# Performance work log

Measured on AMD Instinct MI355X. Metric: run time of the kernel, lower is better.

The kernel has to match this reference:

```python
import jax, jax.numpy as jnp
import numpy as np

H = 12          # num_attention_heads
DH = 64         # attention_head_size
EPS = 1e-12     # F.normalize eps
MAX_LOG_SCALE = float(np.log(1.0 / 0.01))  # clamp max for logit_scale


def _l2norm(x):
    # F.normalize(x, dim=-1): x / max(||x||_2, eps)
    n = jnp.sqrt(jnp.sum(x * x, axis=-1, keepdims=True))
    return x / jnp.maximum(n, EPS)


def setup_inputs() -> dict:
    key = jax.random.key(0)
    ks = jax.random.split(key, 9)
    B, S, D = 4, 2048, 768
    sd = 1.0 / np.sqrt(D)
    inp = {
        "hidden_states": jax.random.normal(ks[0], (B, S, D), jnp.float32),
        "Wq": jax.random.normal(ks[1], (D, D), jnp.float32) * sd,
        "bq": jnp.zeros((D,), jnp.float32),
        "Wk": jax.random.normal(ks[2], (D, D), jnp.float32) * sd,
        "bk": jnp.zeros((D,), jnp.float32),
        "Wv": jax.random.normal(ks[3], (D, D), jnp.float32) * sd,
        "bv": jnp.zeros((D,), jnp.float32),
        "Wo": jax.random.normal(ks[4], (D, D), jnp.float32) * sd,
        "bo": jnp.zeros((D,), jnp.float32),
        "logit_scale": jnp.log(10.0 * jnp.ones((H, 1, 1), jnp.float32)),
    }
    return inp


def reference(hidden_states, Wq, bq, Wk, bk, Wv, bv, Wo, bo, logit_scale):
    B, S, D = hidden_states.shape
    # QKV projections (torch Linear: x @ W.T + b), split heads -> [B,H,S,DH]
    def proj(W, b):
        y = hidden_states @ W.T + b
        return y.reshape(B, S, H, DH).transpose(0, 2, 1, 3)
    q = proj(Wq, bq)
    k = proj(Wk, bk)
    v = proj(Wv, bv)
    # cosine-similarity scores scaled by clamped-exp per-head logit scale
    scale = jnp.exp(jnp.minimum(logit_scale, MAX_LOG_SCALE))  # [H,1,1]
    scores = jnp.einsum('bhqd,bhkd->bhqk', _l2norm(q), _l2norm(k)) * scale[None]
    probs = jax.nn.softmax(scores, axis=-1)
    ctx = jnp.einsum('bhqk,bhkd->bhqd', probs, v)
    ctx = ctx.transpose(0, 2, 1, 3).reshape(B, S, D)
    return ctx @ Wo.T + bo
```

## Files before the change

kernel.cpp:

```cpp
#include <hip/hip_runtime.h>
#include <math.h>

#define Hh 12
#define S_LEN 2048
#define D_MODEL 768
#define HD 64

static constexpr float MAXLS = 4.6051701859880914f;
static constexpr float LOG2E = 1.4426950408889634f;

typedef short bf16x8 __attribute__((ext_vector_type(8)));
typedef float f32x4  __attribute__((ext_vector_type(4)));
typedef float f32x16 __attribute__((ext_vector_type(16)));
typedef unsigned short u16x4 __attribute__((ext_vector_type(4)));
typedef unsigned short u16x8 __attribute__((ext_vector_type(8)));
typedef unsigned int u32x4 __attribute__((ext_vector_type(4)));

__device__ __forceinline__ unsigned short f2bf(float x) {
    unsigned int u = __builtin_bit_cast(unsigned int, x);
    unsigned int r = (u + 0x7FFF + ((u >> 16) & 1)) >> 16;
    return (unsigned short)r;
}

__device__ __forceinline__ unsigned int cvtpk(float a, float b) {
    unsigned int r;
    asm("v_cvt_pk_bf16_f32 %0, %1, %2" : "=v"(r) : "v"(a), "v"(b));
    return r;
}

__device__ __forceinline__ void gload16(const void* g, void* l) {
    __builtin_amdgcn_global_load_lds(
        (const __attribute__((address_space(1))) unsigned int*)g,
        (__attribute__((address_space(3))) unsigned int*)l, 16, 0, 0);
}

__global__ __launch_bounds__(256)
void convert_bf16(const float* __restrict__ hs,
                  const float* __restrict__ Wq, const float* __restrict__ Wk,
                  const float* __restrict__ Wv, const float* __restrict__ Wo,
                  unsigned short* __restrict__ hsb,
                  unsigned short* __restrict__ wqkvb,
                  unsigned short* __restrict__ wob)
{
    const long long N0 = 8192LL * 768;
    const long long NW = 768LL * 768;
    const long long e  = ((long long)blockIdx.x * 256 + threadIdx.x) * 8;
    const float* src; unsigned short* dst;
    if (e < N0) { src = hs + e; dst = hsb + e; }
    else if (e < N0 + 3*NW) {
        const long long r = e - N0;
        const int z = (int)(r / NW);
        src = (z == 0 ? Wq : z == 1 ? Wk : Wv) + (r - (long long)z * NW);
        dst = wqkvb + r;
    } else {
        const long long r = e - N0 - 3*NW;
        src = Wo + r; dst = wob + r;
    }
    const float4 f0 = *(const float4*)src;
    const float4 f1 = *(const float4*)(src + 4);
    u16x8 o;
    o[0]=f2bf(f0.x); o[1]=f2bf(f0.y); o[2]=f2bf(f0.z); o[3]=f2bf(f0.w);
    o[4]=f2bf(f1.x); o[5]=f2bf(f1.y); o[6]=f2bf(f1.z); o[7]=f2bf(f1.w);
    *(u16x8*)dst = o;
}

template<int MODE, int BN, int NWGX>
__global__ __launch_bounds__(256)
void gemm_bf16(const unsigned short* __restrict__ A,
               const unsigned short* __restrict__ Wt,
               const float* __restrict__ b0, const float* __restrict__ b1,
               const float* __restrict__ b2, const float* __restrict__ ls,
               unsigned short* __restrict__ qb, unsigned short* __restrict__ kb,
               unsigned short* __restrict__ vt, float* __restrict__ out)
{
    constexpr int K  = 768;
    constexpr int JW = BN / 32;
    __shared__ char As[16384];
    __shared__ char Bs[BN * 128];

    constexpr int CPX = (NWGX * 64) / 8;
    const int bid = blockIdx.x;
    const int wg  = (bid & 7) * CPX + (bid >> 3);
    const int n0  = (wg % NWGX) * BN;
    const int m0  = (wg / NWGX) * 128;

    const int tid = threadIdx.x, w = tid >> 6, l = tid & 63;
    const int wr = w >> 1, wc = w & 1, hi = l >> 4, ll = l & 15;

    const int srow = l >> 3;
    const int sch  = (l & 7) ^ srow;
    const char* Ab = (const char*)(A  + (size_t)(m0 + w*32) * K) + srow * (K*2) + sch * 16;
    const char* Bb = (const char*)(Wt + (size_t)(n0 + w*(BN/4)) * K) + srow * (K*2) + sch * 16;
    char* AsW = As + (w*32) * 128;
    char* BsW = Bs + (w*(BN/4)) * 128;

    f32x4 acc[4][JW];
    #pragma unroll
    for (int i = 0; i < 4; ++i)
        #pragma unroll
        for (int j = 0; j < JW; ++j) acc[i][j] = (f32x4){0.f,0.f,0.f,0.f};

    for (int kt = 0; kt < K/64; ++kt) {
        __syncthreads();
        #pragma unroll
        for (int s = 0; s < 4; ++s)
            gload16(Ab + kt*128 + s*8*(K*2), AsW + s*1024);
        #pragma unroll
        for (int s = 0; s < JW; ++s)
            gload16(Bb + kt*128 + s*8*(K*2), BsW + s*1024);
        __syncthreads();

        bf16x8 af[2][4], bf[2][JW];
        #pragma unroll
        for (int kk = 0; kk < 2; ++kk) {
            const int pc = kk*4 + hi;
            #pragma unroll
            for (int i = 0; i < 4; ++i) {
                const int ra = wr*64 + i*16 + ll;
                af[kk][i] = *(const bf16x8*)(As + ra*128 + ((pc ^ (ra & 7)) << 4));
            }
            #pragma unroll
            for (int j = 0; j < JW; ++j) {
                const int rb = wc*(BN/2) + j*16 + ll;
                bf[kk][j] = *(const bf16x8*)(Bs + rb*128 + ((pc ^ (rb & 7)) << 4));
            }
        }
        #pragma unroll
        for (int kk = 0; kk < 2; ++kk)
            #pragma unroll
            for (int i = 0; i < 4; ++i)
                #pragma unroll
                for (int j = 0; j < JW; ++j)
                    acc[i][j] = __builtin_amdgcn_mfma_f32_16x16x32_bf16(af[kk][i], bf[kk][j], acc[i][j], 0, 0, 0);
    }

    if (MODE == 0) {
        const int z  = n0 / 768;
        const int nl = (n0 % 768) + wc*64;
        const int h  = nl >> 6;
        const int b  = m0 >> 11;
        const int s0 = (m0 & (S_LEN-1)) + wr*64;
        const float* bias = (z == 0) ? b0 : (z == 1) ? b1 : b2;
        float bj[4];
        #pragma unroll
        for (int j = 0; j < 4; ++j) bj[j] = bias[nl + j*16 + ll];

        if (z < 2) {
            const float sc = (z == 0) ? expf(fminf(ls[h], MAXLS)) * LOG2E : 1.0f;
            unsigned short* dst = (z == 0 ? qb : kb) + ((size_t)(b*Hh + h) * S_LEN) * HD;
            #pragma unroll
            for (int i = 0; i < 4; ++i) {
                float vv[4][4]; float ss[4] = {0.f, 0.f, 0.f, 0.f};
                #pragma unroll
                for (int r = 0; r < 4; ++r)
                    #pragma unroll
                    for (int j = 0; j < 4; ++j) {
                        const float x = acc[i][j][r] + bj[j];
                        vv[r][j] = x; ss[r] += x * x;
                    }
                #pragma unroll
                for (int mm = 1; mm < 16; mm <<= 1) {
                    ss[0] += __shfl_xor(ss[0], mm, 64);
                    ss[1] += __shfl_xor(ss[1], mm, 64);
                    ss[2] += __shfl_xor(ss[2], mm, 64);
                    ss[3] += __shfl_xor(ss[3], mm, 64);
                }
                #pragma unroll
                for (int r = 0; r < 4; ++r) {
                    const float inv = sc / fmaxf(sqrtf(ss[r]), 1e-12f);
                    const int s = s0 + i*16 + hi*4 + r;
                    u16x4 o;
                    #pragma unroll
                    for (int j = 0; j < 4; ++j) o[j] = f2bf(vv[r][j] * inv);
                    *(u16x4*)(dst + (size_t)s * HD + ll*4) = o;
                }
            }
        } else {
            __syncthreads();
            char* T = (w < 2 ? As : Bs) + (w & 1) * 8192;
            const int ch_add = hi & 1;
            const int half8  = hi >> 1;
            #pragma unroll
            for (int j = 0; j < 4; ++j) {
                const int d = j*16 + ll;
                #pragma unroll
                for (int i = 0; i < 4; ++i) {
                    u16x4 o;
                    #pragma unroll
                    for (int r = 0; r < 4; ++r) o[r] = f2bf(acc[i][j][r] + bj[j]);
                    const int byteoff = d*128 + (((i*2 + ch_add) ^ (d & 7)) << 4) + half8*8;
                    *(u16x4*)(T + byteoff) = o;
                }
            }
            const int dl = l >> 2;
            #pragma unroll
            for (int dp = 0; dp < 4; ++dp) {
                const int d = dp*16 + dl;
                unsigned short* vrow = vt + ((size_t)(b*Hh + h) * HD + d) * S_LEN + s0;
                #pragma unroll
                for (int rep = 0; rep < 2; ++rep) {
                    const int c = (l & 3) + rep*4;
                    const u16x8 vv = *(const u16x8*)(T + d*128 + ((c ^ (d & 7)) << 4));
                    *(u16x8*)(vrow + c*8) = vv;
                }
            }
        }
    } else {
        #pragma unroll
        for (int i = 0; i < 4; ++i)
            #pragma unroll
            for (int j = 0; j < JW; ++j) {
                const int n = n0 + wc*(BN/2) + j*16 + ll;
                const float bn = b0[n];
                #pragma unroll
                for (int r = 0; r < 4; ++r) {
                    const int m = m0 + wr*64 + i*16 + hi*4 + r;
                    out[(size_t)m * D_MODEL + n] = acc[i][j][r] + bn;
                }
            }
    }
}

__global__ __launch_bounds__(256, 4)
void attn_mfma5(const char* __restrict__ qb_, const char* __restrict__ kb_,
                const char* __restrict__ vtb_,
                unsigned short* __restrict__ ctx)
{
    __shared__ char smem[49152];
    constexpr int NT = S_LEN / 64;

    const int flat = blockIdx.x;
    const int xcd = flat & 7, ix = flat >> 3;
    const int bh = xcd * 6 + (ix >> 4);
    const int q0 = (ix & 15) * 128;
    const int b = bh / Hh, h = bh % Hh;

    const int tid = threadIdx.x, w = tid >> 6, l = tid & 63;
    const int lq = l & 31, g = l >> 5;

    const char* qg = qb_ + ((size_t)bh * S_LEN + q0 + w * 32) * 128;
    const char* kg = kb_ + (size_t)bh * S_LEN * 128 + (size_t)l * 128;
    const char* vg = vtb_ + (size_t)bh * HD * (S_LEN * 2) + (size_t)l * 4096;

    bf16x8 qf[4];
    #pragma unroll
    for (int s = 0; s < 4; ++s)
        qf[s] = *(const bf16x8*)(qg + lq * 128 + s * 32 + g * 16);

    const short oneb = (short)0x3F80;
    const bf16x8 onesf = {oneb, oneb, oneb, oneb, oneb, oneb, oneb, oneb};

    f32x16 acco0, acco1, accl;
    #pragma unroll
    for (int i = 0; i < 16; ++i) { acco0[i] = 0.f; acco1[i] = 0.f; accl[i] = 0.f; }

#define STAGE(bi, kt) do {                                                   \
        char* dstS = smem + ((bi) << 14);                                    \
        gload16(kg + (size_t)(kt) * 8192 + w * 16,        dstS + w * 1024);          \
        gload16(kg + (size_t)(kt) * 8192 + (w+4) * 16,    dstS + (w+4) * 1024);      \
        gload16(vg + (size_t)(kt) * 128 + w * 16,         dstS + 8192 + w * 1024);   \
        gload16(vg + (size_t)(kt) * 128 + (w+4) * 16,     dstS + 8192 + (w+4) * 1024); \
    } while (0)

    auto qk = [&](const char* Ks, f32x16& o0, f32x16& o1) {
        __builtin_amdgcn_s_setprio(1);
        #pragma unroll
        for (int s = 0; s < 4; ++s) {
            const bf16x8 kf0 = *(const bf16x8*)(Ks + (2*s + g) * 1024 + lq * 16);
            o0 = __builtin_amdgcn_mfma_f32_32x32x16_bf16(kf0, qf[s], o0, 0, 0, 0);
            const bf16x8 kf1 = *(const bf16x8*)(Ks + (2*s + g) * 1024 + 512 + lq * 16);
            o1 = __builtin_amdgcn_mfma_f32_32x32x16_bf16(kf1, qf[s], o1, 0, 0, 0);
        }
        __builtin_amdgcn_s_setprio(0);
    };

    auto softmax_pv = [&](const f32x16& s0v, const f32x16& s1v, const char* Vs) {
        #pragma unroll
        for (int t = 0; t < 4; ++t) {
            float p[8];
            #pragma unroll
            for (int e = 0; e < 8; ++e) {
                const float sv = (t & 2) ? s1v[8*(t&1) + e] : s0v[8*(t&1) + e];
                p[e] = __builtin_amdgcn_exp2f(sv);
            }
            u32x4 pu;
            pu[0] = cvtpk(p[0], p[1]);
            pu[1] = cvtpk(p[2], p[3]);
            pu[2] = cvtpk(p[4], p[5]);
            pu[3] = cvtpk(p[6], p[7]);
            const bf16x8 pa = __builtin_bit_cast(bf16x8, pu);

            __builtin_amdgcn_s_setprio(1);
            const bf16x8 vf0 = *(const bf16x8*)(Vs + (2*t + g) * 1024 + lq * 16);
            acco0 = __builtin_amdgcn_mfma_f32_32x32x16_bf16(pa, vf0, acco0, 0, 0, 0);
            const bf16x8 vf1 = *(const bf16x8*)(Vs + (2*t + g) * 1024 + 512 + lq * 16);
            acco1 = __builtin_amdgcn_mfma_f32_32x32x16_bf16(pa, vf1, acco1, 0, 0, 0);
            accl  = __builtin_amdgcn_mfma_f32_32x32x16_bf16(pa, onesf, accl, 0, 0, 0);
            __builtin_amdgcn_s_setprio(0);
        }
    };

    STAGE(0, 0);
    __syncthreads();
    STAGE(1, 1);
    f32x16 sa0c, sa1c;
    #pragma unroll
    for (int i = 0; i < 16; ++i) { sa0c[i] = 0.f; sa1c[i] = 0.f; }
    qk(smem, sa0c, sa1c);
    __syncthreads();

    int bc = 0, bn = 1, bs = 2;
    #pragma unroll 3
    for (int kt = 0; kt < NT - 1; ++kt) {
        if (kt + 2 < NT) STAGE(bs, kt + 2);
        f32x16 sa0n, sa1n;
        #pragma unroll
        for (int i = 0; i < 16; ++i) { sa0n[i] = 0.f; sa1n[i] = 0.f; }
        qk(smem + (bn << 14), sa0n, sa1n);
        softmax_pv(sa0c, sa1c, smem + (bc << 14) + 8192);
        __syncthreads();
        sa0c = sa0n; sa1c = sa1n;
        const int t0 = bc; bc = bn; bn = bs; bs = t0;
    }
    softmax_pv(sa0c, sa1c, smem + (bc << 14) + 8192);
#undef STAGE

    #pragma unroll
    for (int r = 0; r < 16; ++r) {
        const int qrow = (r & 3) + 8 * (r >> 2) + 4 * g;
        const float inv = 1.0f / accl[r];
        unsigned short* crow = ctx + ((size_t)b * S_LEN + q0 + w * 32 + qrow) * D_MODEL + h * HD;
        crow[lq]      = f2bf(acco0[r] * inv);
        crow[32 + lq] = f2bf(acco1[r] * inv);
    }
}

extern "C" void kernel_launch(void* const* d_in, const int* in_sizes, int n_in,
                              void* d_out, int out_size, void* d_ws, size_t ws_size,
                              hipStream_t stream)
{
    const float* hs = (const float*)d_in[0];
    const float* Wq = (const float*)d_in[1];
    const float* bq = (const float*)d_in[2];
    const float* Wk = (const float*)d_in[3];
    const float* bk = (const float*)d_in[4];
    const float* Wv = (const float*)d_in[5];
    const float* bv = (const float*)d_in[6];
    const float* Wo = (const float*)d_in[7];
    const float* bo = (const float*)d_in[8];
    const float* ls = (const float*)d_in[9];
    float* out = (float*)d_out;

    const int B = 4;
    const size_t nHS = 8192ULL * 768;
    const size_t nW  = 768ULL * 768;
    const size_t nPB = (size_t)B * Hh * S_LEN * HD;

    unsigned short* hsb   = (unsigned short*)d_ws;
    unsigned short* wqkvb = hsb + nHS;
    unsigned short* wob   = wqkvb + 3 * nW;
    unsigned short* qbuf  = wob + nW;
    unsigned short* kbuf  = qbuf + nPB;
    unsigned short* vtb   = kbuf + nPB;
    unsigned short* cbuf  = vtb + nPB;

    hipLaunchKernelGGL(convert_bf16, dim3(4224), dim3(256), 0, stream,
                       hs, Wq, Wk, Wv, Wo, hsb, wqkvb, wob);

    hipLaunchKernelGGL((gemm_bf16<0, 128, 18>), dim3(18 * 64), dim3(256), 0, stream,
                       hsb, wqkvb, bq, bk, bv, ls, qbuf, kbuf, vtb, nullptr);

    hipLaunchKernelGGL(attn_mfma5, dim3((S_LEN/128) * B * Hh), dim3(256), 0, stream,
                       (const char*)qbuf, (const char*)kbuf, (const char*)vtb, cbuf);

    hipLaunchKernelGGL((gemm_bf16<1, 64, 12>), dim3(12 * 64), dim3(256), 0, stream,
                       cbuf, wob, bo, nullptr, nullptr, nullptr,
                       nullptr, nullptr, nullptr, out);
}
```

Before: 214.8 us.

## Give each attention wave 64 query rows and compute row sums in VALU

The attention kernel now runs 2 waves of 64 query rows each instead of 4 waves of 32. Each K/V fragment read from LDS therefore feeds twice as many MFMAs. The extra ones-vector MFMA that produced softmax denominators is replaced by VALU sums of the probabilities, combined across lane halves with shuffles. The 3-buffer software pipeline that overlapped the next QK with the current softmax/PV becomes a plain 2-buffer loop. This lowers per-block wave count and register headroom, and may expose more latency.

```diff
diff --git a/kernel.cpp b/kernel.cpp
--- a/kernel.cpp
+++ b/kernel.cpp
@@ -221,12 +221,12 @@
     }
 }
 
-__global__ __launch_bounds__(256, 4)
-void attn_mfma5(const char* __restrict__ qb_, const char* __restrict__ kb_,
+__global__ __launch_bounds__(128, 2)
+void attn_mfma6(const char* __restrict__ qb_, const char* __restrict__ kb_,
                 const char* __restrict__ vtb_,
                 unsigned short* __restrict__ ctx)
 {
-    __shared__ char smem[49152];
+    __shared__ char smem[32768];
     constexpr int NT = S_LEN / 64;
 
     const int flat = blockIdx.x;
@@ -238,100 +238,107 @@
     const int tid = threadIdx.x, w = tid >> 6, l = tid & 63;
     const int lq = l & 31, g = l >> 5;
 
-    const char* qg = qb_ + ((size_t)bh * S_LEN + q0 + w * 32) * 128;
+    const char* qg = qb_ + ((size_t)bh * S_LEN + q0 + w * 64) * 128;
     const char* kg = kb_ + (size_t)bh * S_LEN * 128 + (size_t)l * 128;
     const char* vg = vtb_ + (size_t)bh * HD * (S_LEN * 2) + (size_t)l * 4096;
 
-    bf16x8 qf[4];
+    bf16x8 qf0[4], qf1[4];
     #pragma unroll
-    for (int s = 0; s < 4; ++s)
-        qf[s] = *(const bf16x8*)(qg + lq * 128 + s * 32 + g * 16);
-
-    const short oneb = (short)0x3F80;
-    const bf16x8 onesf = {oneb, oneb, oneb, oneb, oneb, oneb, oneb, oneb};
-
-    f32x16 acco0, acco1, accl;
+    for (int s = 0; s < 4; ++s) {
+        qf0[s] = *(const bf16x8*)(qg + (size_t)lq * 128 + s * 32 + g * 16);
+        qf1[s] = *(const bf16x8*)(qg + (size_t)(32 + lq) * 128 + s * 32 + g * 16);
+    }
+
+    f32x16 acc00, acc01, acc10, acc11;
     #pragma unroll
-    for (int i = 0; i < 16; ++i) { acco0[i] = 0.f; acco1[i] = 0.f; accl[i] = 0.f; }
-
-#define STAGE(bi, kt) do {                                                   \
-        char* dstS = smem + ((bi) << 14);                                    \
-        gload16(kg + (size_t)(kt) * 8192 + w * 16,        dstS + w * 1024);          \
-        gload16(kg + (size_t)(kt) * 8192 + (w+4) * 16,    dstS + (w+4) * 1024);      \
-        gload16(vg + (size_t)(kt) * 128 + w * 16,         dstS + 8192 + w * 1024);   \
-        gload16(vg + (size_t)(kt) * 128 + (w+4) * 16,     dstS + 8192 + (w+4) * 1024); \
+    for (int i = 0; i < 16; ++i) { acc00[i]=0.f; acc01[i]=0.f; acc10[i]=0.f; acc11[i]=0.f; }
+    float lsum0 = 0.f, lsum1 = 0.f;
+
+#define STAGE(bi, kt) do {                                                    \
+        char* dS = smem + ((bi) << 14);                                       \
+        gload16(kg + (size_t)(kt)*8192 + (4*w+0)*16, dS + (4*w+0)*1024);      \
+        gload16(kg + (size_t)(kt)*8192 + (4*w+1)*16, dS + (4*w+1)*1024);      \
+        gload16(kg + (size_t)(kt)*8192 + (4*w+2)*16, dS + (4*w+2)*1024);      \
+        gload16(kg + (size_t)(kt)*8192 + (4*w+3)*16, dS + (4*w+3)*1024);      \
+        gload16(vg + (size_t)(kt)*128 + (4*w+0)*16, dS + 8192 + (4*w+0)*1024);\
+        gload16(vg + (size_t)(kt)*128 + (4*w+1)*16, dS + 8192 + (4*w+1)*1024);\
+        gload16(vg + (size_t)(kt)*128 + (4*w+2)*16, dS + 8192 + (4*w+2)*1024);\
+        gload16(vg + (size_t)(kt)*128 + (4*w+3)*16, dS + 8192 + (4*w+3)*1024);\
     } while (0)
 
-    auto qk = [&](const char* Ks, f32x16& o0, f32x16& o1) {
+    STAGE(0, 0);
+    __syncthreads();
+    int cur = 0;
+
+    for (int kt = 0; kt < NT; ++kt) {
+        if (kt + 1 < NT) STAGE(cur ^ 1, kt + 1);
+        const char* Ks = smem + (cur << 14);
+        const char* Vs = Ks + 8192;
+
+        f32x16 sa00, sa01, sa10, sa11;
+        #pragma unroll
+        for (int i = 0; i < 16; ++i) { sa00[i]=0.f; sa01[i]=0.f; sa10[i]=0.f; sa11[i]=0.f; }
+
         __builtin_amdgcn_s_setprio(1);
         #pragma unroll
         for (int s = 0; s < 4; ++s) {
             const bf16x8 kf0 = *(const bf16x8*)(Ks + (2*s + g) * 1024 + lq * 16);
-            o0 = __builtin_amdgcn_mfma_f32_32x32x16_bf16(kf0, qf[s], o0, 0, 0, 0);
             const bf16x8 kf1 = *(const bf16x8*)(Ks + (2*s + g) * 1024 + 512 + lq * 16);
-            o1 = __builtin_amdgcn_mfma_f32_32x32x16_bf16(kf1, qf[s], o1, 0, 0, 0);
+            sa00 = __builtin_amdgcn_mfma_f32_32x32x16_bf16(kf0, qf0[s], sa00, 0, 0, 0);
+            sa01 = __builtin_amdgcn_mfma_f32_32x32x16_bf16(kf0, qf1[s], sa01, 0, 0, 0);
+            sa10 = __builtin_amdgcn_mfma_f32_32x32x16_bf16(kf1, qf0[s], sa10, 0, 0, 0);
+            sa11 = __builtin_amdgcn_mfma_f32_32x32x16_bf16(kf1, qf1[s], sa11, 0, 0, 0);
         }
         __builtin_amdgcn_s_setprio(0);
-    };
-
-    auto softmax_pv = [&](const f32x16& s0v, const f32x16& s1v, const char* Vs) {
+
         #pragma unroll
         for (int t = 0; t < 4; ++t) {
-            float p[8];
+            float p0[8], p1[8];
             #pragma unroll
             for (int e = 0; e < 8; ++e) {
-                const float sv = (t & 2) ? s1v[8*(t&1) + e] : s0v[8*(t&1) + e];
-                p[e] = __builtin_amdgcn_exp2f(sv);
-            }
-            u32x4 pu;
-            pu[0] = cvtpk(p[0], p[1]);
-            pu[1] = cvtpk(p[2], p[3]);
-            pu[2] = cvtpk(p[4], p[5]);
-            pu[3] = cvtpk(p[6], p[7]);
-            const bf16x8 pa = __builtin_bit_cast(bf16x8, pu);
-
+                const float s0v = (t & 2) ? sa10[8*(t&1) + e] : sa00[8*(t&1) + e];
+                const float s1v = (t & 2) ? sa11[8*(t&1) + e] : sa01[8*(t&1) + e];
+                p0[e] = __builtin_amdgcn_exp2f(s0v);
+                p1[e] = __builtin_amdgcn_exp2f(s1v);
+            }
+            lsum0 += ((p0[0]+p0[1]) + (p0[2]+p0[3])) + ((p0[4]+p0[5]) + (p0[6]+p0[7]));
+            lsum1 += ((p1[0]+p1[1]) + (p1[2]+p1[3])) + ((p1[4]+p1[5]) + (p1[6]+p1[7]));
+            u32x4 u0, u1;
+            u0[0] = cvtpk(p0[0], p0[1]); u0[1] = cvtpk(p0[2], p0[3]);
+            u0[2] = cvtpk(p0[4], p0[5]); u0[3] = cvtpk(p0[6], p0[7]);
+            u1[0] = cvtpk(p1[0], p1[1]); u1[1] = cvtpk(p1[2], p1[3]);
+            u1[2] = cvtpk(p1[4], p1[5]); u1[3] = cvtpk(p1[6], p1[7]);
+            const bf16x8 pa0 = __builtin_bit_cast(bf16x8, u0);
+            const bf16x8 pa1 = __builtin_bit_cast(bf16x8, u1);
+
+            const bf16x8 vf0 = *(const bf16x8*)(Vs + (2*t + g) * 1024 + lq * 16);
+            const bf16x8 vf1 = *(const bf16x8*)(Vs + (2*t + g) * 1024 + 512 + lq * 16);
             __builtin_amdgcn_s_setprio(1);
-            const bf16x8 vf0 = *(const bf16x8*)(Vs + (2*t + g) * 1024 + lq * 16);
-            acco0 = __builtin_amdgcn_mfma_f32_32x32x16_bf16(pa, vf0, acco0, 0, 0, 0);
-            const bf16x8 vf1 = *(const bf16x8*)(Vs + (2*t + g) * 1024 + 512 + lq * 16);
-            acco1 = __builtin_amdgcn_mfma_f32_32x32x16_bf16(pa, vf1, acco1, 0, 0, 0);
-            accl  = __builtin_amdgcn_mfma_f32_32x32x16_bf16(pa, onesf, accl, 0, 0, 0);
+            acc00 = __builtin_amdgcn_mfma_f32_32x32x16_bf16(pa0, vf0, acc00, 0, 0, 0);
+            acc01 = __builtin_amdgcn_mfma_f32_32x32x16_bf16(pa0, vf1, acc01, 0, 0, 0);
+            acc10 = __builtin_amdgcn_mfma_f32_32x32x16_bf16(pa1, vf0, acc10, 0, 0, 0);
+            acc11 = __builtin_amdgcn_mfma_f32_32x32x16_bf16(pa1, vf1, acc11, 0, 0, 0);
             __builtin_amdgcn_s_setprio(0);
         }
-    };
-
-    STAGE(0, 0);
-    __syncthreads();
-    STAGE(1, 1);
-    f32x16 sa0c, sa1c;
-    #pragma unroll
-    for (int i = 0; i < 16; ++i) { sa0c[i] = 0.f; sa1c[i] = 0.f; }
-    qk(smem, sa0c, sa1c);
-    __syncthreads();
-
-    int bc = 0, bn = 1, bs = 2;
-    #pragma unroll 3
-    for (int kt = 0; kt < NT - 1; ++kt) {
-        if (kt + 2 < NT) STAGE(bs, kt + 2);
-        f32x16 sa0n, sa1n;
-        #pragma unroll
-        for (int i = 0; i < 16; ++i) { sa0n[i] = 0.f; sa1n[i] = 0.f; }
-        qk(smem + (bn << 14), sa0n, sa1n);
-        softmax_pv(sa0c, sa1c, smem + (bc << 14) + 8192);
+
         __syncthreads();
-        sa0c = sa0n; sa1c = sa1n;
-        const int t0 = bc; bc = bn; bn = bs; bs = t0;
-    }
-    softmax_pv(sa0c, sa1c, smem + (bc << 14) + 8192);
+        cur ^= 1;
+    }
 #undef STAGE
 
+    lsum0 += __shfl_xor(lsum0, 32, 64);
+    lsum1 += __shfl_xor(lsum1, 32, 64);
     #pragma unroll
     for (int r = 0; r < 16; ++r) {
         const int qrow = (r & 3) + 8 * (r >> 2) + 4 * g;
-        const float inv = 1.0f / accl[r];
-        unsigned short* crow = ctx + ((size_t)b * S_LEN + q0 + w * 32 + qrow) * D_MODEL + h * HD;
-        crow[lq]      = f2bf(acco0[r] * inv);
-        crow[32 + lq] = f2bf(acco1[r] * inv);
+        const float i0 = 1.0f / __shfl(lsum0, qrow, 64);
+        const float i1 = 1.0f / __shfl(lsum1, qrow, 64);
+        unsigned short* c0 = ctx + ((size_t)b * S_LEN + q0 + w * 64 + qrow) * D_MODEL + h * HD;
+        unsigned short* c1 = ctx + ((size_t)b * S_LEN + q0 + w * 64 + 32 + qrow) * D_MODEL + h * HD;
+        c0[lq]      = f2bf(acc00[r] * i0);
+        c0[32 + lq] = f2bf(acc01[r] * i0);
+        c1[lq]      = f2bf(acc10[r] * i1);
+        c1[32 + lq] = f2bf(acc11[r] * i1);
     }
 }
 
@@ -370,7 +377,7 @@
     hipLaunchKernelGGL((gemm_bf16<0, 128, 18>), dim3(18 * 64), dim3(256), 0, stream,
                        hsb, wqkvb, bq, bk, bv, ls, qbuf, kbuf, vtb, nullptr);
 
-    hipLaunchKernelGGL(attn_mfma5, dim3((S_LEN/128) * B * Hh), dim3(256), 0, stream,
+    hipLaunchKernelGGL(attn_mfma6, dim3((S_LEN/128) * B * Hh), dim3(128), 0, stream,
                        (const char*)qbuf, (const char*)kbuf, (const char*)vtb, cbuf);
 
     hipLaunchKernelGGL((gemm_bf16<1, 64, 12>), dim3(12 * 64), dim3(256), 0, stream,
```

After: 220.9 us. 2.8% more time.
